# Performance work log

Hardware: AMD Instinct MI355X
Metric: run time of the kernel (lower is better)

## Reference

```python
import jax, jax.numpy as jnp
import numpy as np

DIM = 2048
HEADS = 16
HD = DIM // HEADS  # 128
EPS = 1e-5


def layernorm(t, w, b):
    # FloatLayerNorm: LayerNorm computed in float32 over last dim
    t32 = t.astype(jnp.float32)
    mu = jnp.mean(t32, axis=-1, keepdims=True)
    var = jnp.mean(jnp.square(t32 - mu), axis=-1, keepdims=True)
    y = (t32 - mu) * jax.lax.rsqrt(var + EPS)
    return (y * w + b).astype(t.dtype)


def rope(t, f_real, f_imag):
    # t: [b, s, h, hd]; frequencies in cis form, sliced to seq length
    b, s, h, hd = t.shape
    tr = t.astype(jnp.float32).reshape(b, s, h, hd // 2, 2)
    xr, xi = tr[..., 0], tr[..., 1]
    fr = f_real[:s][None, :, None, :]  # [1, s, 1, hd/2]
    fi = f_imag[:s][None, :, None, :]
    o_r = xr * fr - xi * fi
    o_i = xr * fi + xi * fr
    return jnp.stack([o_r, o_i], axis=-1).reshape(b, s, h, hd).astype(t.dtype)


def proj_norm_rope(t, Wq, Wk, Wv, qn_w, qn_b, kn_w, kn_b, f_real, f_imag):
    b, s, _ = t.shape
    q = layernorm(t @ Wq, qn_w, qn_b).reshape(b, s, HEADS, HD)
    k = layernorm(t @ Wk, kn_w, kn_b).reshape(b, s, HEADS, HD)
    v = (t @ Wv).reshape(b, s, HEADS, HD)
    q = rope(q, f_real, f_imag)
    k = rope(k, f_real, f_imag)
    return q, k, v


def sdpa(q, k, v, scale):
    # q,k,v: [b, s, h, hd] -> out [b, s, h, hd]
    scores = jnp.einsum('bqhd,bkhd->bhqk', q, k) * scale
    probs = jax.nn.softmax(scores, axis=-1)
    return jnp.einsum('bhqk,bkhd->bqhd', probs, v)


def setup_inputs() -> dict:
    key = jax.random.key(0)
    ks = jax.random.split(key, 14)
    d = {
        'c': jax.random.normal(ks[0], (2, 256, DIM), jnp.float32),
        'x': jax.random.normal(ks[1], (2, 1792, DIM), jnp.float32),
        'f_real': jax.random.normal(ks[2], (2048, HD // 2), jnp.float32),
        'f_imag': jax.random.normal(ks[3], (2048, HD // 2), jnp.float32),
    }
    sc = 1.0 / np.sqrt(DIM)
    for i, name in enumerate(['Wq', 'Wk', 'Wv', 'Wo', 'W2q', 'W2k', 'W2v', 'W2o']):
        d[name] = jax.random.normal(ks[4 + i], (DIM, DIM), jnp.float32) * sc
    for name in ['qn_w', 'kn_w', 'q2n_w', 'k2n_w']:
        d[name] = jnp.ones((DIM,), jnp.float32)
    for name in ['qn_b', 'kn_b', 'q2n_b', 'k2n_b']:
        d[name] = jnp.zeros((DIM,), jnp.float32)
    return d


def reference(c, x, f_real, f_imag, Wq, Wk, Wv, Wo, W2q, W2k, W2v, W2o,
              qn_w, qn_b, kn_w, kn_b, q2n_w, q2n_b, k2n_w, k2n_b):
    s1 = c.shape[1]
    c_q, c_k, c_v = proj_norm_rope(c, Wq, Wk, Wv, qn_w, qn_b, kn_w, kn_b, f_real, f_imag)
    x_q, x_k, x_v = proj_norm_rope(x, W2q, W2k, W2v, q2n_w, q2n_b, k2n_w, k2n_b, f_real, f_imag)
    q = jnp.concatenate([c_q, x_q], axis=1)
    k = jnp.concatenate([c_k, x_k], axis=1)
    v = jnp.concatenate([c_v, x_v], axis=1)
    out = sdpa(q, k, v, scale=1.0 / np.sqrt(HD))  # scale_by_num_heads=True
    b, s, _, _ = out.shape
    out = out.reshape(b, s, DIM)
    c_out = out[:, :s1] @ Wo
    x_out = out[:, s1:] @ W2o
    return c_out, x_out
```

## Files before the change

kernel.cpp:

```cpp
#include <hip/hip_runtime.h>

typedef __attribute__((ext_vector_type(8))) short short8;
typedef __attribute__((ext_vector_type(4))) float f32x4;
typedef __attribute__((ext_vector_type(16))) float f32x16;

#define DEV __device__ __forceinline__

DEV unsigned short f2bf(float f) {
  unsigned int u; __builtin_memcpy(&u, &f, 4);
  u = (u + 0x7FFFu + ((u >> 16) & 1u)) >> 16;
  return (unsigned short)u;
}
DEV float bf2f(unsigned short h) {
  unsigned int u = ((unsigned int)h) << 16;
  float f; __builtin_memcpy(&f, &u, 4);
  return f;
}
DEV unsigned int cvtpk(float lo, float hi_) {
  unsigned int r;
  asm("v_cvt_pk_bf16_f32 %0, %1, %2" : "=v"(r) : "v"(lo), "v"(hi_));
  return r;
}

DEV void gload_lds16(const void* g, void* l) {
  __builtin_amdgcn_global_load_lds(
      (const __attribute__((address_space(1))) void*)g,
      (__attribute__((address_space(3))) void*)l, 16, 0, 0);
}

DEV f32x16 mfma32(short8 a, short8 b, f32x16 c) {
  return __builtin_amdgcn_mfma_f32_32x32x16_bf16(a, b, c, 0, 0, 0);
}
DEV f32x4 mfma16(short8 a, short8 b, f32x4 c) {
  return __builtin_amdgcn_mfma_f32_16x16x32_bf16(a, b, c, 0, 0, 0);
}

__global__ __launch_bounds__(256) void conv_tb(const float* __restrict__ c,
                                               const float* __restrict__ x,
                                               unsigned short* __restrict__ tb) {
  int row = blockIdx.x;
  int b = row >> 11, s = row & 2047;
  const float* src = (s < 256) ? (c + (size_t)(b * 256 + s) * 2048)
                               : (x + (size_t)(b * 1792 + (s - 256)) * 2048);
  int t = threadIdx.x;
  float4 v0 = *(const float4*)&src[t * 8];
  float4 v1 = *(const float4*)&src[t * 8 + 4];
  union { unsigned short us[8]; uint4 u; } pk;
  pk.us[0] = f2bf(v0.x); pk.us[1] = f2bf(v0.y); pk.us[2] = f2bf(v0.z); pk.us[3] = f2bf(v0.w);
  pk.us[4] = f2bf(v1.x); pk.us[5] = f2bf(v1.y); pk.us[6] = f2bf(v1.z); pk.us[7] = f2bf(v1.w);
  *(uint4*)&tb[(size_t)row * 2048 + t * 8] = pk.u;
}

__global__ __launch_bounds__(256) void trans_w(
    const float* __restrict__ w0, const float* __restrict__ w1,
    const float* __restrict__ w2, const float* __restrict__ w3,
    const float* __restrict__ w4, const float* __restrict__ w5,
    const float* __restrict__ w6, const float* __restrict__ w7,
    unsigned short* __restrict__ dstbase) {
  const float* W;
  switch (blockIdx.z) {
    case 0: W = w0; break; case 1: W = w1; break; case 2: W = w2; break; case 3: W = w3; break;
    case 4: W = w4; break; case 5: W = w5; break; case 6: W = w6; break; default: W = w7; break;
  }
  unsigned short* Wt = dstbase + (size_t)blockIdx.z * 2048 * 2048;
  __shared__ float tile[64][65];
  int n0 = blockIdx.x * 64, k0 = blockIdx.y * 64;
  int j = threadIdx.x & 63, i0 = threadIdx.x >> 6;
#pragma unroll
  for (int p = 0; p < 16; ++p) {
    int i = i0 + p * 4;
    tile[i][j] = W[(size_t)(k0 + i) * 2048 + n0 + j];
  }
  __syncthreads();
#pragma unroll
  for (int p = 0; p < 16; ++p) {
    int i = i0 + p * 4;
    Wt[(size_t)(n0 + i) * 2048 + k0 + j] = f2bf(tile[j][i]);
  }
}

DEV void stage_A8(char* ldsAbase, const unsigned short* gtile, int mh, int wid, int lane) {
#pragma unroll
  for (int p = 0; p < 2; ++p) {
    int row0 = mh * 64 + p * 128 + wid * 8;
    int row = row0 + (lane >> 3);
    int u = (lane & 7) ^ (row & 7);
    gload_lds16(gtile + (size_t)row * 2048 + u * 8, ldsAbase + row0 * 128);
  }
}
DEV void stage_B8(char* ldsBbase, const unsigned short* gtile, int nh, int wid, int lane) {
#pragma unroll
  for (int p = 0; p < 2; ++p) {
    int idx = p * 8 + wid;
    int row0 = (idx >> 2) * 64 + nh * 32 + (idx & 3) * 8;
    int row = row0 + (lane >> 3);
    int u = (lane & 7) ^ (row & 7);
    gload_lds16(gtile + (size_t)row * 2048 + u * 8, ldsBbase + row0 * 128);
  }
}

__global__ __launch_bounds__(512, 2) void gemm_qkv3_8ph(
    const unsigned short* __restrict__ A,
    const unsigned short* __restrict__ Wt,
    unsigned short* __restrict__ out) {
  extern __shared__ __align__(16) char ldsc[];
  const size_t M2 = 2048ull * 2048ull;
  int bid = blockIdx.x;
  int sw = (bid & 7) * 48 + (bid >> 3);
  const int which = sw >> 7;
  const int rem = sw & 127;
  const int m0 = (rem >> 3) * 256, n0 = (rem & 7) * 256;
  const unsigned short* Bt = Wt + (size_t)(((m0 & 2047) < 256) ? which : which + 4) * M2;
  unsigned short* C = out + (size_t)which * (4096ull * 2048ull);
  const int tid = threadIdx.x, wid = tid >> 6, lane = tid & 63;
  const int g = lane >> 4, l15 = lane & 15;
  const int wm = wid >> 2, wn = wid & 3;
  const unsigned short* gA = A + (size_t)m0 * 2048;
  const unsigned short* gB = Bt + (size_t)n0 * 2048;

  f32x4 acc[8][4] = {};

  stage_A8(ldsc, gA, 0, wid, lane);
  stage_A8(ldsc, gA, 1, wid, lane);
  stage_B8(ldsc + 32768, gB, 0, wid, lane);
  stage_B8(ldsc + 32768, gB, 1, wid, lane);
  stage_A8(ldsc + 65536, gA + 64, 0, wid, lane);
  stage_B8(ldsc + 98304, gB + 64, 0, wid, lane);
  asm volatile("s_waitcnt vmcnt(4)" ::: "memory");
  __builtin_amdgcn_s_barrier();

  const int NT = 32;
#pragma unroll 1
  for (int t = 0; t < NT; ++t) {
    const int bufOff = (t & 1) << 16;
    char* Ab = ldsc + bufOff;
    char* Bb = ldsc + 32768 + bufOff;
    char* An = ldsc + (bufOff ^ 65536);
    char* Bn = ldsc + 32768 + (bufOff ^ 65536);
    short8 af[4][2], bf0[2][2], bf1[2][2];

#pragma unroll
    for (int m4 = 0; m4 < 4; ++m4)
#pragma unroll
      for (int k2 = 0; k2 < 2; ++k2) {
        int row = wm * 128 + m4 * 16 + l15;
        af[m4][k2] = *(const short8*)(Ab + row * 128 + (((k2 * 4 + g) ^ (row & 7)) << 4));
      }
#pragma unroll
    for (int n2 = 0; n2 < 2; ++n2)
#pragma unroll
      for (int k2 = 0; k2 < 2; ++k2) {
        int row = wn * 64 + n2 * 16 + l15;
        bf0[n2][k2] = *(const short8*)(Bb + row * 128 + (((k2 * 4 + g) ^ (row & 7)) << 4));
      }
    if (t + 1 < NT) stage_B8(Bn, gB + (t + 1) * 64, 1, wid, lane);
    __builtin_amdgcn_s_barrier();
    asm volatile("s_waitcnt lgkmcnt(0)" ::: "memory");
    __builtin_amdgcn_sched_barrier(0);
    __builtin_amdgcn_s_setprio(1);
#pragma unroll
    for (int m4 = 0; m4 < 4; ++m4)
#pragma unroll
      for (int n2 = 0; n2 < 2; ++n2)
#pragma unroll
        for (int k2 = 0; k2 < 2; ++k2)
          acc[m4][n2] = mfma16(af[m4][k2], bf0[n2][k2], acc[m4][n2]);
    __builtin_amdgcn_s_setprio(0);
    __builtin_amdgcn_s_barrier();

#pragma unroll
    for (int n2 = 0; n2 < 2; ++n2)
#pragma unroll
      for (int k2 = 0; k2 < 2; ++k2) {
        int row = wn * 64 + 32 + n2 * 16 + l15;
        bf1[n2][k2] = *(const short8*)(Bb + row * 128 + (((k2 * 4 + g) ^ (row & 7)) << 4));
      }
    if (t + 1 < NT) stage_A8(An, gA + (t + 1) * 64, 1, wid, lane);
    __builtin_amdgcn_s_barrier();
    asm volatile("s_waitcnt lgkmcnt(0)" ::: "memory");
    __builtin_amdgcn_sched_barrier(0);
    __builtin_amdgcn_s_setprio(1);
#pragma unroll
    for (int m4 = 0; m4 < 4; ++m4)
#pragma unroll
      for (int n2 = 0; n2 < 2; ++n2)
#pragma unroll
        for (int k2 = 0; k2 < 2; ++k2)
          acc[m4][2 + n2] = mfma16(af[m4][k2], bf1[n2][k2], acc[m4][2 + n2]);
    __builtin_amdgcn_s_setprio(0);
    __builtin_amdgcn_s_barrier();

#pragma unroll
    for (int m4 = 0; m4 < 4; ++m4)
#pragma unroll
      for (int k2 = 0; k2 < 2; ++k2) {
        int row = wm * 128 + 64 + m4 * 16 + l15;
        af[m4][k2] = *(const short8*)(Ab + row * 128 + (((k2 * 4 + g) ^ (row & 7)) << 4));
      }
    if (t + 2 < NT) stage_A8(Ab, gA + (t + 2) * 64, 0, wid, lane);
    __builtin_amdgcn_s_barrier();
    asm volatile("s_waitcnt lgkmcnt(0)" ::: "memory");
    __builtin_amdgcn_sched_barrier(0);
    __builtin_amdgcn_s_setprio(1);
#pragma unroll
    for (int m4 = 0; m4 < 4; ++m4)
#pragma unroll
      for (int n2 = 0; n2 < 2; ++n2)
#pragma unroll
        for (int k2 = 0; k2 < 2; ++k2)
          acc[4 + m4][n2] = mfma16(af[m4][k2], bf0[n2][k2], acc[4 + m4][n2]);
    __builtin_amdgcn_s_setprio(0);
    __builtin_amdgcn_s_barrier();

    if (t + 2 < NT) stage_B8(Bb, gB + (t + 2) * 64, 0, wid, lane);
    __builtin_amdgcn_s_barrier();
    __builtin_amdgcn_s_setprio(1);
#pragma unroll
    for (int m4 = 0; m4 < 4; ++m4)
#pragma unroll
      for (int n2 = 0; n2 < 2; ++n2)
#pragma unroll
        for (int k2 = 0; k2 < 2; ++k2)
          acc[4 + m4][2 + n2] = mfma16(af[m4][k2], bf1[n2][k2], acc[4 + m4][2 + n2]);
    __builtin_amdgcn_s_setprio(0);
    if (t + 2 < NT) {
      asm volatile("s_waitcnt vmcnt(4)" ::: "memory");
    } else if (t + 1 < NT) {
      asm volatile("s_waitcnt vmcnt(0)" ::: "memory");
    }
    __builtin_amdgcn_s_barrier();
  }

#pragma unroll
  for (int mh = 0; mh < 2; ++mh)
#pragma unroll
    for (int m4 = 0; m4 < 4; ++m4)
#pragma unroll
      for (int r = 0; r < 4; ++r) {
        int row = m0 + wm * 128 + mh * 64 + m4 * 16 + 4 * g + r;
#pragma unroll
        for (int nh = 0; nh < 2; ++nh)
#pragma unroll
          for (int n2 = 0; n2 < 2; ++n2)
            C[(size_t)row * 2048 + n0 + wn * 64 + nh * 32 + n2 * 16 + l15] =
                f2bf(acc[mh * 4 + m4][nh * 2 + n2][r]);
      }
}

__global__ __launch_bounds__(256) void gemm_out(
    const unsigned short* __restrict__ A,
    const unsigned short* __restrict__ B1t,
    const unsigned short* __restrict__ B2t,
    float* __restrict__ Co) {
  __shared__ __align__(16) unsigned short As[128 * 32];
  __shared__ __align__(16) unsigned short Bs[128 * 32];
  const int m0 = blockIdx.y * 128, n0 = blockIdx.x * 128;
  const unsigned short* Bt = ((m0 & 2047) < 256) ? B1t : B2t;
  const int tid = threadIdx.x, wid = tid >> 6, lane = tid & 63;
  const int g = lane >> 4, l15 = lane & 15;
  const int wm = wid >> 1, wn = wid & 1;
  const int srow = lane >> 2, skk = (lane & 3) * 8;
  f32x4 acc[4][4] = {};
  for (int k0 = 0; k0 < 2048; k0 += 32) {
#pragma unroll
    for (int rep = 0; rep < 2; ++rep) {
      int ia = wid * 2 + rep;
      gload_lds16(&A[(size_t)(m0 + ia * 16 + srow) * 2048 + k0 + skk], (char*)As + ia * 1024);
      gload_lds16(&Bt[(size_t)(n0 + ia * 16 + srow) * 2048 + k0 + skk], (char*)Bs + ia * 1024);
    }
    __syncthreads();
    short8 a[4], bb[4];
#pragma unroll
    for (int mf = 0; mf < 4; ++mf) a[mf] = *(const short8*)&As[(wm * 64 + mf * 16 + l15) * 32 + g * 8];
#pragma unroll
    for (int nf = 0; nf < 4; ++nf) bb[nf] = *(const short8*)&Bs[(wn * 64 + nf * 16 + l15) * 32 + g * 8];
#pragma unroll
    for (int mf = 0; mf < 4; ++mf)
#pragma unroll
      for (int nf = 0; nf < 4; ++nf)
        acc[mf][nf] = mfma16(a[mf], bb[nf], acc[mf][nf]);
    __syncthreads();
  }
#pragma unroll
  for (int mf = 0; mf < 4; ++mf)
#pragma unroll
    for (int r = 0; r < 4; ++r) {
      int row = m0 + wm * 64 + mf * 16 + 4 * g + r;
      int b = row >> 11, s = row & 2047;
      size_t dst = (s < 256) ? ((size_t)b * 256 + s) * 2048
                             : 1048576ull + ((size_t)b * 1792 + (s - 256)) * 2048;
#pragma unroll
      for (int nf = 0; nf < 4; ++nf)
        Co[dst + n0 + wn * 64 + nf * 16 + l15] = acc[mf][nf][r];
    }
}

__global__ __launch_bounds__(256) void ln_rope(
    const unsigned short* __restrict__ P,
    const float* __restrict__ w1, const float* __restrict__ b1,
    const float* __restrict__ w2, const float* __restrict__ b2,
    const float* __restrict__ fre, const float* __restrict__ fim,
    unsigned short* __restrict__ Oa, float oscale) {
  int row = blockIdx.x;
  int b = row >> 11, s = row & 2047;
  int pos = (s < 256) ? s : s - 256;
  const float* w = (s < 256) ? w1 : w2;
  const float* bb = (s < 256) ? b1 : b2;
  int t = threadIdx.x, lane = t & 63, wid = t >> 6;
  int col = t * 8;
  uint4 raw = *(const uint4*)&P[(size_t)row * 2048 + col];
  const unsigned short* rp = (const unsigned short*)&raw;
  float xv[8];
#pragma unroll
  for (int j = 0; j < 8; ++j) xv[j] = bf2f(rp[j]);
  float s1 = 0.f, s2 = 0.f;
#pragma unroll
  for (int j = 0; j < 8; ++j) { s1 += xv[j]; s2 += xv[j] * xv[j]; }
#pragma unroll
  for (int off = 32; off; off >>= 1) { s1 += __shfl_xor(s1, off); s2 += __shfl_xor(s2, off); }
  __shared__ float red1[4], red2[4];
  if (lane == 0) { red1[wid] = s1; red2[wid] = s2; }
  __syncthreads();
  s1 = red1[0] + red1[1] + red1[2] + red1[3];
  s2 = red2[0] + red2[1] + red2[2] + red2[3];
  float mean = s1 * (1.f / 2048.f);
  float var = s2 * (1.f / 2048.f) - mean * mean;
  float rs = rsqrtf(var + 1e-5f);
  float4 wv0 = *(const float4*)&w[col], wv1 = *(const float4*)&w[col + 4];
  float4 bv0 = *(const float4*)&bb[col], bv1 = *(const float4*)&bb[col + 4];
  float y[8];
  y[0] = (xv[0] - mean) * rs * wv0.x + bv0.x; y[1] = (xv[1] - mean) * rs * wv0.y + bv0.y;
  y[2] = (xv[2] - mean) * rs * wv0.z + bv0.z; y[3] = (xv[3] - mean) * rs * wv0.w + bv0.w;
  y[4] = (xv[4] - mean) * rs * wv1.x + bv1.x; y[5] = (xv[5] - mean) * rs * wv1.y + bv1.y;
  y[6] = (xv[6] - mean) * rs * wv1.z + bv1.z; y[7] = (xv[7] - mean) * rs * wv1.w + bv1.w;
#pragma unroll
  for (int j = 0; j < 8; ++j) y[j] *= oscale;
  int hd0 = col & 127;
  int i0 = hd0 >> 1;
  float4 fr = *(const float4*)&fre[(size_t)pos * 64 + i0];
  float4 fi = *(const float4*)&fim[(size_t)pos * 64 + i0];
  union { unsigned short us[8]; uint4 u; } pk;
  pk.us[0] = f2bf(y[0] * fr.x - y[1] * fi.x); pk.us[1] = f2bf(y[0] * fi.x + y[1] * fr.x);
  pk.us[2] = f2bf(y[2] * fr.y - y[3] * fi.y); pk.us[3] = f2bf(y[2] * fi.y + y[3] * fr.y);
  pk.us[4] = f2bf(y[4] * fr.z - y[5] * fi.z); pk.us[5] = f2bf(y[4] * fi.z + y[5] * fr.z);
  pk.us[6] = f2bf(y[6] * fr.w - y[7] * fi.w); pk.us[7] = f2bf(y[6] * fi.w + y[7] * fr.w);
  int h = col >> 7;
  *(uint4*)&Oa[((size_t)(b * 16 + h) * 2048 + s) * 128 + hd0] = pk.u;
}

__global__ __launch_bounds__(256) void v_trans(const unsigned short* __restrict__ vp,
                                               unsigned short* __restrict__ va) {
  int bh = blockIdx.y;
  int b = bh >> 4, h = bh & 15;
  int s0 = blockIdx.x * 64;
  __shared__ unsigned short tile[64][128];
  int tid = threadIdx.x;
#pragma unroll
  for (int p = 0; p < 4; ++p) {
    int s = p * 16 + (tid >> 4);
    int d0 = (tid & 15) * 8;
    *(uint4*)&tile[s][d0] = *(const uint4*)&vp[((size_t)b * 2048 + s0 + s) * 2048 + h * 128 + d0];
  }
  __syncthreads();
#pragma unroll
  for (int p = 0; p < 4; ++p) {
    int d = p * 32 + (tid >> 3);
    int soff = (tid & 7) * 8;
    union { unsigned short us[8]; uint4 u; } pk;
#pragma unroll
    for (int u = 0; u < 8; ++u) pk.us[u] = tile[soff + u][d];
    *(uint4*)&va[((size_t)(b * 16 + h) * 128 + d) * 2048 + s0 + soff] = pk.u;
  }
}

#define THR_LOG2 11.5f

__global__ __launch_bounds__(512) void attn_kernel(
    const unsigned short* __restrict__ Q,
    const unsigned short* __restrict__ Kb,
    const unsigned short* __restrict__ Vt,
    unsigned short* __restrict__ O) {
  extern __shared__ __align__(16) char asmem[];
  const int q0 = blockIdx.x * 256;
  const int h = blockIdx.y, b = blockIdx.z;
  const int tid = threadIdx.x, wid = tid >> 6, lane = tid & 63;
  const int l31 = lane & 31, hi = lane >> 5;
  const size_t base = (size_t)(b * 16 + h) * 2048 * 128;
  const unsigned short* kbase = Kb + base;
  const unsigned short* vbase = Vt + base;

  const int qrow = q0 + wid * 32 + l31;
  short8 qf[8];
#pragma unroll
  for (int ks = 0; ks < 8; ++ks)
    qf[ks] = *(const short8*)&Q[base + (size_t)qrow * 128 + ks * 16 + hi * 8];

  f32x16 o_acc[4] = {};
  float m_run = -1e30f, l_run = 0.f;

#define STAGE(bufi, kv0)                                                             \
  {                                                                                  \
_Pragma("unroll")                                                                    \
    for (int p = 0; p < 2; ++p) {                                                    \
      int slot = p * 512 + wid * 64 + lane;                                          \
      int row = slot >> 4;                                                           \
      int u = (slot & 15) ^ (row & 7);                                               \
      gload_lds16(&kbase[(size_t)((kv0) + row) * 128 + u * 8],                       \
                  asmem + (bufi) * 32768 + (p * 512 + wid * 64) * 16);               \
    }                                                                                \
_Pragma("unroll")                                                                    \
    for (int p = 0; p < 2; ++p) {                                                    \
      int slot = p * 512 + wid * 64 + lane;                                          \
      int d = slot >> 3;                                                             \
      int u = (slot & 7) ^ (d & 7);                                                  \
      gload_lds16(&vbase[(size_t)d * 2048 + (kv0) + u * 8],                          \
                  asmem + (bufi) * 32768 + 16384 + (p * 512 + wid * 64) * 16);       \
    }                                                                                \
  }

  STAGE(0, 0)
  STAGE(1, 64)

#pragma unroll 1
  for (int t = 0; t < 32; ++t) {
    if (t + 2 < 32) {
      STAGE((t + 2) & 3, (t + 2) * 64)
      asm volatile("s_waitcnt vmcnt(8)" ::: "memory");
    } else if (t + 1 < 32) {
      asm volatile("s_waitcnt vmcnt(4)" ::: "memory");
    } else {
      asm volatile("s_waitcnt vmcnt(0)" ::: "memory");
    }
    __builtin_amdgcn_s_barrier();

    const char* Ksb = asmem + (t & 3) * 32768;
    const char* Vsb = Ksb + 16384;

    f32x16 sT0 = {}, sT1 = {};
    __builtin_amdgcn_s_setprio(1);
#pragma unroll
    for (int ks = 0; ks < 8; ++ks) {
      int unit = ks * 2 + hi;
      int r0 = l31;
      short8 kf0 = *(const short8*)(Ksb + ((r0 * 16 + (unit ^ (r0 & 7))) << 4));
      sT0 = mfma32(kf0, qf[ks], sT0);
      int r1 = 32 + l31;
      short8 kf1 = *(const short8*)(Ksb + ((r1 * 16 + (unit ^ (r1 & 7))) << 4));
      sT1 = mfma32(kf1, qf[ks], sT1);
    }
    __builtin_amdgcn_s_setprio(0);

    float mx = sT0[0];
#pragma unroll
    for (int r = 1; r < 16; ++r) mx = fmaxf(mx, sT0[r]);
#pragma unroll
    for (int r = 0; r < 16; ++r) mx = fmaxf(mx, sT1[r]);
    mx = fmaxf(mx, __shfl_xor(mx, 32));
    if (!__all(mx <= m_run + THR_LOG2)) {
      float mn = fmaxf(m_run, mx);
      float corr = __builtin_exp2f(m_run - mn);
      m_run = mn;
      l_run *= corr;
#pragma unroll
      for (int di = 0; di < 4; ++di)
#pragma unroll
        for (int r = 0; r < 16; ++r) o_acc[di][r] *= corr;
    }
    float ts = 0.f;
#pragma unroll
    for (int r = 0; r < 16; ++r) { sT0[r] = __builtin_exp2f(sT0[r] - m_run); ts += sT0[r]; }
#pragma unroll
    for (int r = 0; r < 16; ++r) { sT1[r] = __builtin_exp2f(sT1[r] - m_run); ts += sT1[r]; }
    ts += __shfl_xor(ts, 32);
    l_run += ts;

    unsigned int w0[8], w1[8];
#pragma unroll
    for (int j = 0; j < 8; ++j) {
      w0[j] = cvtpk(sT0[2 * j], sT0[2 * j + 1]);
      w1[j] = cvtpk(sT1[2 * j], sT1[2 * j + 1]);
    }
    unsigned int y0[4], y1[4];
    y0[0] = __shfl_xor((int)(hi ? w0[0] : w0[2]), 32);
    y0[1] = __shfl_xor((int)(hi ? w0[1] : w0[3]), 32);
    y0[2] = __shfl_xor((int)(hi ? w0[4] : w0[6]), 32);
    y0[3] = __shfl_xor((int)(hi ? w0[5] : w0[7]), 32);
    y1[0] = __shfl_xor((int)(hi ? w1[0] : w1[2]), 32);
    y1[1] = __shfl_xor((int)(hi ? w1[1] : w1[3]), 32);
    y1[2] = __shfl_xor((int)(hi ? w1[4] : w1[6]), 32);
    y1[3] = __shfl_xor((int)(hi ? w1[5] : w1[7]), 32);
    union { unsigned int u[4]; short8 s8; } pf[2][2];
    pf[0][0].u[0] = hi ? y0[0] : w0[0]; pf[0][0].u[1] = hi ? y0[1] : w0[1];
    pf[0][0].u[2] = hi ? w0[2] : y0[0]; pf[0][0].u[3] = hi ? w0[3] : y0[1];
    pf[0][1].u[0] = hi ? y0[2] : w0[4]; pf[0][1].u[1] = hi ? y0[3] : w0[5];
    pf[0][1].u[2] = hi ? w0[6] : y0[2]; pf[0][1].u[3] = hi ? w0[7] : y0[3];
    pf[1][0].u[0] = hi ? y1[0] : w1[0]; pf[1][0].u[1] = hi ? y1[1] : w1[1];
    pf[1][0].u[2] = hi ? w1[2] : y1[0]; pf[1][0].u[3] = hi ? w1[3] : y1[1];
    pf[1][1].u[0] = hi ? y1[2] : w1[4]; pf[1][1].u[1] = hi ? y1[3] : w1[5];
    pf[1][1].u[2] = hi ? w1[6] : y1[2]; pf[1][1].u[3] = hi ? w1[7] : y1[3];

    __builtin_amdgcn_s_setprio(1);
#pragma unroll
    for (int di = 0; di < 4; ++di) {
      int row = di * 32 + l31;
      int sw = row & 7;
#pragma unroll
      for (int kb = 0; kb < 2; ++kb)
#pragma unroll
        for (int ks2 = 0; ks2 < 2; ++ks2) {
          int unit = kb * 4 + ks2 * 2 + hi;
          short8 vf = *(const short8*)(Vsb + ((row * 8 + (unit ^ sw)) << 4));
          o_acc[di] = mfma32(vf, pf[kb][ks2].s8, o_acc[di]);
        }
    }
    __builtin_amdgcn_s_setprio(0);
  }

  float inv = 1.0f / l_run;
  char* ow = asmem + wid * 8192;
#pragma unroll
  for (int di = 0; di < 4; ++di)
#pragma unroll
    for (int rg = 0; rg < 4; ++rg) {
      unsigned int lo = cvtpk(o_acc[di][rg * 4 + 0] * inv, o_acc[di][rg * 4 + 1] * inv);
      unsigned int hi_w = cvtpk(o_acc[di][rg * 4 + 2] * inv, o_acc[di][rg * 4 + 3] * inv);
      int byte = (l31 * 256 + di * 64 + rg * 16 + hi * 8) ^ ((l31 & 7) << 4);
      *(unsigned long long*)(ow + byte) =
          ((unsigned long long)hi_w << 32) | (unsigned long long)lo;
    }
  asm volatile("s_waitcnt lgkmcnt(0)" ::: "memory");
  size_t obase = ((size_t)b * 2048 + q0 + wid * 32) * 2048 + (size_t)h * 128;
#pragma unroll
  for (int it = 0; it < 8; ++it) {
    int q = it * 4 + (lane >> 4);
    int d0 = (lane & 15) * 8;
    int byte = (q * 256 + d0 * 2) ^ ((q & 7) << 4);
    uint4 val = *(const uint4*)(ow + byte);
    *(uint4*)&O[obase + (size_t)q * 2048 + d0] = val;
  }
}

extern "C" void kernel_launch(void* const* d_in, const int* in_sizes, int n_in,
                              void* d_out, int out_size, void* d_ws, size_t ws_size,
                              hipStream_t stream) {
  (void)in_sizes; (void)n_in; (void)out_size; (void)ws_size;
  const float* c = (const float*)d_in[0];
  const float* x = (const float*)d_in[1];
  const float* fre = (const float*)d_in[2];
  const float* fim = (const float*)d_in[3];

  char* ws = (char*)d_ws;
  const size_t M2 = 2048ull * 2048ull;
  unsigned short* tb = (unsigned short*)ws;
  unsigned short* Wt = (unsigned short*)(ws + 16777216ull);
  unsigned short* qkv = (unsigned short*)(ws + 83886080ull);
  unsigned short* qp = qkv;
  unsigned short* kp = (unsigned short*)(ws + 100663296ull);
  unsigned short* vp = (unsigned short*)(ws + 117440512ull);
  unsigned short* qa = (unsigned short*)(ws + 134217728ull);
  unsigned short* ka = (unsigned short*)(ws + 150994944ull);
  unsigned short* va = (unsigned short*)(ws + 167772160ull);
  unsigned short* attn_out = qp;

  (void)hipFuncSetAttribute((const void*)gemm_qkv3_8ph,
                            hipFuncAttributeMaxDynamicSharedMemorySize, 131072);
  (void)hipFuncSetAttribute((const void*)attn_kernel,
                            hipFuncAttributeMaxDynamicSharedMemorySize, 131072);

  conv_tb<<<4096, 256, 0, stream>>>(c, x, tb);
  trans_w<<<dim3(32, 32, 8), 256, 0, stream>>>(
      (const float*)d_in[4], (const float*)d_in[5], (const float*)d_in[6], (const float*)d_in[7],
      (const float*)d_in[8], (const float*)d_in[9], (const float*)d_in[10], (const float*)d_in[11],
      Wt);
  gemm_qkv3_8ph<<<384, 512, 131072, stream>>>(tb, Wt, qkv);
  ln_rope<<<4096, 256, 0, stream>>>(qp, (const float*)d_in[12], (const float*)d_in[16],
                                    (const float*)d_in[14], (const float*)d_in[18], fre, fim, qa,
                                    0.08838834764831845f * 1.4426950408889634f);
  ln_rope<<<4096, 256, 0, stream>>>(kp, (const float*)d_in[13], (const float*)d_in[17],
                                    (const float*)d_in[15], (const float*)d_in[19], fre, fim, ka,
                                    1.0f);
  v_trans<<<dim3(32, 32), 256, 0, stream>>>(vp, va);
  attn_kernel<<<dim3(8, 16, 2), 512, 131072, stream>>>(qa, ka, va, attn_out);
  gemm_out<<<dim3(16, 32), 256, 0, stream>>>(attn_out, Wt + 3 * M2, Wt + 7 * M2, (float*)d_out);
}
```

Baseline: 349.8 us.

## Restructure QKV GEMM pipeline into two phases and merge q/k LN-RoPE launches

```diff
diff --git a/kernel.cpp b/kernel.cpp
--- a/kernel.cpp
+++ b/kernel.cpp
@@ -119,6 +119,7 @@
   const unsigned short* gB = Bt + (size_t)n0 * 2048;
 
   f32x4 acc[8][4] = {};
+  short8 af[4][2], bf0[2][2], bf1[2][2];
 
   stage_A8(ldsc, gA, 0, wid, lane);
   stage_A8(ldsc, gA, 1, wid, lane);
@@ -126,7 +127,8 @@
   stage_B8(ldsc + 32768, gB, 1, wid, lane);
   stage_A8(ldsc + 65536, gA + 64, 0, wid, lane);
   stage_B8(ldsc + 98304, gB + 64, 0, wid, lane);
-  asm volatile("s_waitcnt vmcnt(4)" ::: "memory");
+  stage_B8(ldsc + 98304, gB + 64, 1, wid, lane);
+  asm volatile("s_waitcnt vmcnt(6)" ::: "memory");
   __builtin_amdgcn_s_barrier();
 
   const int NT = 32;
@@ -136,8 +138,6 @@
     char* Ab = ldsc + bufOff;
     char* Bb = ldsc + 32768 + bufOff;
     char* An = ldsc + (bufOff ^ 65536);
-    char* Bn = ldsc + 32768 + (bufOff ^ 65536);
-    short8 af[4][2], bf0[2][2], bf1[2][2];
 
 #pragma unroll
     for (int m4 = 0; m4 < 4; ++m4)
@@ -153,21 +153,6 @@
         int row = wn * 64 + n2 * 16 + l15;
         bf0[n2][k2] = *(const short8*)(Bb + row * 128 + (((k2 * 4 + g) ^ (row & 7)) << 4));
       }
-    if (t + 1 < NT) stage_B8(Bn, gB + (t + 1) * 64, 1, wid, lane);
-    __builtin_amdgcn_s_barrier();
-    asm volatile("s_waitcnt lgkmcnt(0)" ::: "memory");
-    __builtin_amdgcn_sched_barrier(0);
-    __builtin_amdgcn_s_setprio(1);
-#pragma unroll
-    for (int m4 = 0; m4 < 4; ++m4)
-#pragma unroll
-      for (int n2 = 0; n2 < 2; ++n2)
-#pragma unroll
-        for (int k2 = 0; k2 < 2; ++k2)
-          acc[m4][n2] = mfma16(af[m4][k2], bf0[n2][k2], acc[m4][n2]);
-    __builtin_amdgcn_s_setprio(0);
-    __builtin_amdgcn_s_barrier();
-
 #pragma unroll
     for (int n2 = 0; n2 < 2; ++n2)
 #pragma unroll
@@ -183,11 +168,20 @@
 #pragma unroll
     for (int m4 = 0; m4 < 4; ++m4)
 #pragma unroll
-      for (int n2 = 0; n2 < 2; ++n2)
-#pragma unroll
-        for (int k2 = 0; k2 < 2; ++k2)
+      for (int k2 = 0; k2 < 2; ++k2) {
+#pragma unroll
+        for (int n2 = 0; n2 < 2; ++n2)
+          acc[m4][n2] = mfma16(af[m4][k2], bf0[n2][k2], acc[m4][n2]);
+#pragma unroll
+        for (int n2 = 0; n2 < 2; ++n2)
           acc[m4][2 + n2] = mfma16(af[m4][k2], bf1[n2][k2], acc[m4][2 + n2]);
+      }
     __builtin_amdgcn_s_setprio(0);
+    if (t + 1 < NT) {
+      asm volatile("s_waitcnt vmcnt(8)" ::: "memory");
+    } else {
+      asm volatile("s_waitcnt vmcnt(0)" ::: "memory");
+    }
     __builtin_amdgcn_s_barrier();
 
 #pragma unroll
@@ -197,7 +191,11 @@
         int row = wm * 128 + 64 + m4 * 16 + l15;
         af[m4][k2] = *(const short8*)(Ab + row * 128 + (((k2 * 4 + g) ^ (row & 7)) << 4));
       }
-    if (t + 2 < NT) stage_A8(Ab, gA + (t + 2) * 64, 0, wid, lane);
+    if (t + 2 < NT) {
+      stage_A8(Ab, gA + (t + 2) * 64, 0, wid, lane);
+      stage_B8(Bb, gB + (t + 2) * 64, 0, wid, lane);
+      stage_B8(Bb, gB + (t + 2) * 64, 1, wid, lane);
+    }
     __builtin_amdgcn_s_barrier();
     asm volatile("s_waitcnt lgkmcnt(0)" ::: "memory");
     __builtin_amdgcn_sched_barrier(0);
@@ -205,27 +203,18 @@
 #pragma unroll
     for (int m4 = 0; m4 < 4; ++m4)
 #pragma unroll
-      for (int n2 = 0; n2 < 2; ++n2)
-#pragma unroll
-        for (int k2 = 0; k2 < 2; ++k2)
+      for (int k2 = 0; k2 < 2; ++k2) {
+#pragma unroll
+        for (int n2 = 0; n2 < 2; ++n2)
           acc[4 + m4][n2] = mfma16(af[m4][k2], bf0[n2][k2], acc[4 + m4][n2]);
-    __builtin_amdgcn_s_setprio(0);
-    __builtin_amdgcn_s_barrier();
-
-    if (t + 2 < NT) stage_B8(Bb, gB + (t + 2) * 64, 0, wid, lane);
-    __builtin_amdgcn_s_barrier();
-    __builtin_amdgcn_s_setprio(1);
-#pragma unroll
-    for (int m4 = 0; m4 < 4; ++m4)
-#pragma unroll
-      for (int n2 = 0; n2 < 2; ++n2)
-#pragma unroll
-        for (int k2 = 0; k2 < 2; ++k2)
+#pragma unroll
+        for (int n2 = 0; n2 < 2; ++n2)
           acc[4 + m4][2 + n2] = mfma16(af[m4][k2], bf1[n2][k2], acc[4 + m4][2 + n2]);
+      }
     __builtin_amdgcn_s_setprio(0);
     if (t + 2 < NT) {
-      asm volatile("s_waitcnt vmcnt(4)" ::: "memory");
-    } else if (t + 1 < NT) {
+      asm volatile("s_waitcnt vmcnt(8)" ::: "memory");
+    } else {
       asm volatile("s_waitcnt vmcnt(0)" ::: "memory");
     }
     __builtin_amdgcn_s_barrier();
@@ -295,17 +284,24 @@
     }
 }
 
-__global__ __launch_bounds__(256) void ln_rope(
+__global__ __launch_bounds__(256) void ln_rope2(
     const unsigned short* __restrict__ P,
-    const float* __restrict__ w1, const float* __restrict__ b1,
-    const float* __restrict__ w2, const float* __restrict__ b2,
+    const float* __restrict__ qw1, const float* __restrict__ qb1,
+    const float* __restrict__ qw2, const float* __restrict__ qb2,
+    const float* __restrict__ kw1, const float* __restrict__ kb1,
+    const float* __restrict__ kw2, const float* __restrict__ kb2,
     const float* __restrict__ fre, const float* __restrict__ fim,
-    unsigned short* __restrict__ Oa, float oscale) {
-  int row = blockIdx.x;
+    unsigned short* __restrict__ Oa, float qscale) {
+  int gid = blockIdx.x;
+  int mat = gid >> 12;
+  int row = gid & 4095;
+  P += (size_t)mat * 8388608ull;
+  Oa += (size_t)mat * 8388608ull;
+  float oscale = mat ? 1.0f : qscale;
   int b = row >> 11, s = row & 2047;
   int pos = (s < 256) ? s : s - 256;
-  const float* w = (s < 256) ? w1 : w2;
-  const float* bb = (s < 256) ? b1 : b2;
+  const float* w = (s < 256) ? (mat ? kw1 : qw1) : (mat ? kw2 : qw2);
+  const float* bb = (s < 256) ? (mat ? kb1 : qb1) : (mat ? kb2 : qb2);
   int t = threadIdx.x, lane = t & 63, wid = t >> 6;
   int col = t * 8;
   uint4 raw = *(const uint4*)&P[(size_t)row * 2048 + col];
@@ -555,7 +551,6 @@
   unsigned short* Wt = (unsigned short*)(ws + 16777216ull);
   unsigned short* qkv = (unsigned short*)(ws + 83886080ull);
   unsigned short* qp = qkv;
-  unsigned short* kp = (unsigned short*)(ws + 100663296ull);
   unsigned short* vp = (unsigned short*)(ws + 117440512ull);
   unsigned short* qa = (unsigned short*)(ws + 134217728ull);
   unsigned short* ka = (unsigned short*)(ws + 150994944ull);
@@ -573,12 +568,13 @@
       (const float*)d_in[8], (const float*)d_in[9], (const float*)d_in[10], (const float*)d_in[11],
       Wt);
   gemm_qkv3_8ph<<<384, 512, 131072, stream>>>(tb, Wt, qkv);
-  ln_rope<<<4096, 256, 0, stream>>>(qp, (const float*)d_in[12], (const float*)d_in[16],
-                                    (const float*)d_in[14], (const float*)d_in[18], fre, fim, qa,
-                                    0.08838834764831845f * 1.4426950408889634f);
-  ln_rope<<<4096, 256, 0, stream>>>(kp, (const float*)d_in[13], (const float*)d_in[17],
-                                    (const float*)d_in[15], (const float*)d_in[19], fre, fim, ka,
-                                    1.0f);
+  ln_rope2<<<8192, 256, 0, stream>>>(qp,
+                                     (const float*)d_in[12], (const float*)d_in[16],
+                                     (const float*)d_in[14], (const float*)d_in[18],
+                                     (const float*)d_in[13], (const float*)d_in[17],
+                                     (const float*)d_in[15], (const float*)d_in[19],
+                                     fre, fim, qa,
+                                     0.08838834764831845f * 1.4426950408889634f);
   v_trans<<<dim3(32, 32), 256, 0, stream>>>(vp, va);
   attn_kernel<<<dim3(8, 16, 2), 512, 131072, stream>>>(qa, ka, va, attn_out);
   gemm_out<<<dim3(16, 32), 256, 0, stream>>>(attn_out, Wt + 3 * M2, Wt + 7 * M2, (float*)d_out);
```

Result: faster. 339.1 us (-3.1%).
